# Performance work log

Measured on AMD Instinct MI355X. Metric: run time of the kernel, lower is better.

## Reference

```python
import jax, jax.numpy as jnp
import numpy as np

D_MODEL = 384
D_STATE = 64
N_LAYERS = 2
OUTPUT_DIM = 60
MAX_SEQ = 128
EXPAND = 2
D_CONV = 4
HEADDIM = 64
D_INNER = EXPAND * D_MODEL            # 768
NHEADS = D_INNER // HEADDIM           # 12
CONV_DIM = D_INNER + 2 * D_STATE      # 896
D_IN_PROJ = 2 * D_INNER + 2 * D_STATE + NHEADS  # 1676
BATCH = 256
SEQ = 128
EPS = 1e-5


def _pos_encoding(seq_len, d_model):
    pos = np.arange(seq_len, dtype=np.float32)[:, None]
    div = np.exp(np.arange(0, d_model, 2, dtype=np.float32) * (-np.log(10000.0) / d_model))
    pe = np.zeros((seq_len, d_model), dtype=np.float32)
    pe[:, 0::2] = np.sin(pos * div)
    pe[:, 1::2] = np.cos(pos * div)
    return jnp.asarray(pe)


def setup_inputs() -> dict:
    key = jax.random.key(0)
    ks = jax.random.split(key, 16)
    f32 = jnp.float32
    inp = {}
    inp["memory_embeddings"] = jax.random.normal(ks[0], (BATCH, SEQ, D_MODEL), dtype=f32)
    # per-layer Mamba2 params, stacked over layers
    inp["in_proj_w"] = jax.random.normal(ks[1], (N_LAYERS, D_IN_PROJ, D_MODEL), dtype=f32) * 0.02
    inp["conv_w"] = jax.random.normal(ks[2], (N_LAYERS, CONV_DIM, D_CONV), dtype=f32) * 0.2
    inp["conv_b"] = jax.random.normal(ks[3], (N_LAYERS, CONV_DIM), dtype=f32) * 0.02
    inp["dt_bias"] = jax.random.normal(ks[4], (N_LAYERS, NHEADS), dtype=f32) * 0.5 - 4.0
    inp["A_log"] = jnp.log(jax.random.uniform(ks[5], (N_LAYERS, NHEADS), dtype=f32, minval=1.0, maxval=16.0))
    inp["D"] = jnp.ones((N_LAYERS, NHEADS), dtype=f32) + jax.random.normal(ks[6], (N_LAYERS, NHEADS), dtype=f32) * 0.1
    inp["mamba_norm_w"] = jnp.ones((N_LAYERS, D_INNER), dtype=f32)
    inp["out_proj_w"] = jax.random.normal(ks[7], (N_LAYERS, D_MODEL, D_INNER), dtype=f32) * 0.02
    # pre-Mamba LayerNorms
    inp["ln_w"] = jnp.ones((N_LAYERS, D_MODEL), dtype=f32)
    inp["ln_b"] = jnp.zeros((N_LAYERS, D_MODEL), dtype=f32)
    # output norm + projection
    inp["out_norm_w"] = jnp.ones((D_MODEL,), dtype=f32)
    inp["out_norm_b"] = jnp.zeros((D_MODEL,), dtype=f32)
    inp["proj_w"] = jax.random.normal(ks[8], (OUTPUT_DIM, D_MODEL), dtype=f32) * 0.05
    inp["proj_b"] = jnp.zeros((OUTPUT_DIM,), dtype=f32)
    return inp


def _layernorm(x, w, b):
    mu = jnp.mean(x, axis=-1, keepdims=True)
    var = jnp.mean(jnp.square(x - mu), axis=-1, keepdims=True)
    return (x - mu) * jax.lax.rsqrt(var + EPS) * w + b


def _silu(x):
    return x * jax.nn.sigmoid(x)


def _mamba2_block(x, in_proj_w, conv_w, conv_b, dt_bias, A_log, D, norm_w, out_proj_w):
    b, l, _ = x.shape
    zxbcdt = jnp.einsum('bld,ed->ble', x, in_proj_w)  # (b,l,1676)
    z = zxbcdt[..., :D_INNER]
    xBC = zxbcdt[..., D_INNER:D_INNER + CONV_DIM]
    dt = jax.nn.softplus(zxbcdt[..., -NHEADS:] + dt_bias)  # (b,l,h)
    # depthwise causal conv1d (kernel 4) + silu
    xp = jnp.pad(xBC, ((0, 0), (D_CONV - 1, 0), (0, 0)))
    xconv = conv_b
    for k in range(D_CONV):
        xconv = xconv + xp[:, k:k + l, :] * conv_w[:, k]
    xBC = _silu(xconv)
    xh = xBC[..., :D_INNER].reshape(b, l, NHEADS, HEADDIM)  # (b,l,h,p)
    Bm = xBC[..., D_INNER:D_INNER + D_STATE]                # (b,l,n)
    Cm = xBC[..., D_INNER + D_STATE:]                       # (b,l,n)
    A = -jnp.exp(A_log)  # (h,)

    def step(h, inp):
        x_t, B_t, C_t, dt_t = inp  # (b,h,p), (b,n), (b,n), (b,h)
        dA = jnp.exp(dt_t * A)  # (b,h)
        h = h * dA[..., None, None] + jnp.einsum('bh,bhp,bn->bhpn', dt_t, x_t, B_t)
        y = jnp.einsum('bhpn,bn->bhp', h, C_t)
        return h, y

    h0 = jnp.zeros((b, NHEADS, HEADDIM, D_STATE), dtype=x.dtype)
    xs = (xh.transpose(1, 0, 2, 3), Bm.transpose(1, 0, 2), Cm.transpose(1, 0, 2), dt.transpose(1, 0, 2))
    _, ys = jax.lax.scan(step, h0, xs)          # ys: (l,b,h,p)
    y = ys.transpose(1, 0, 2, 3) + D[None, None, :, None] * xh
    y = y.reshape(b, l, D_INNER)
    # gated RMSNorm (norm_before_gate=False): rmsnorm(y * silu(z)) * weight
    g = y * _silu(z)
    g = g * jax.lax.rsqrt(jnp.mean(jnp.square(g), axis=-1, keepdims=True) + EPS) * norm_w
    return jnp.einsum('ble,de->bld', g, out_proj_w)


def reference(memory_embeddings, in_proj_w, conv_w, conv_b, dt_bias, A_log, D,
              mamba_norm_w, out_proj_w, ln_w, ln_b, out_norm_w, out_norm_b,
              proj_w, proj_b):
    b, l, d = memory_embeddings.shape
    pe = _pos_encoding(MAX_SEQ, D_MODEL)[:l]
    x = memory_embeddings + pe[None]  # dropout is identity at eval
    for i in range(N_LAYERS):
        residual = x
        xn = _layernorm(x, ln_w[i], ln_b[i])
        xm = _mamba2_block(xn, in_proj_w[i], conv_w[i], conv_b[i], dt_bias[i],
                           A_log[i], D[i], mamba_norm_w[i], out_proj_w[i])
        x = xm + residual
    x = _layernorm(x, out_norm_w, out_norm_b)
    final = x[:, -1, :]  # (b, d_model)
    return final @ proj_w.T + proj_b  # (b, output_dim)
```

## Files before the change

### kernel.cpp

```cpp
#include <hip/hip_runtime.h>
#include <math.h>

#define BATCH   256
#define SEQ     128
#define DMODEL  384
#define DSTATE  64
#define DINNER  768
#define NHEADS  12
#define HEADDIM 64
#define CONVDIM 896
#define DPROJ   1676
#define N1PAD   1792
#define OUTDIM  60
#define MTOT    (BATCH*SEQ)

typedef unsigned short u16;
typedef unsigned int   u32;
typedef short bf16x8 __attribute__((ext_vector_type(8)));
typedef float f32x4 __attribute__((ext_vector_type(4)));

#define ASG __attribute__((address_space(1)))
#define ASL __attribute__((address_space(3)))

__device__ __forceinline__ float siluf(float x){ return __fdividef(x, 1.f + __expf(-x)); }
__device__ __forceinline__ float softplusf(float x){ return fmaxf(x,0.f) + log1pf(expf(-fabsf(x))); }
__device__ __forceinline__ u16 f2bf(float x){
  union { float f; unsigned int u; } c; c.f = x;
  unsigned int r = c.u + 0x7FFFu + ((c.u >> 16) & 1u);
  return (u16)(r >> 16);
}
__device__ __forceinline__ float bf2f(u16 u){
  union { unsigned int u; float f; } c; c.u = ((unsigned int)u) << 16;
  return c.f;
}

__global__ void add_pe_kernel(const float* __restrict__ emb, float* __restrict__ x){
  int idx = blockIdx.x*256 + threadIdx.x;
  int d = idx % DMODEL;
  int l = (idx / DMODEL) % SEQ;
  int i = d >> 1;
  float div = expf((float)(2*i) * (-9.210340371976184f/384.f));
  float arg = (float)l * div;
  float pe = (d & 1) ? cosf(arg) : sinf(arg);
  x[idx] = emb[idx] + pe;
}

__global__ void wconv_in2_kernel(const float* __restrict__ w, u16* __restrict__ o){
  int idx = blockIdx.x*256 + threadIdx.x;
  int n = idx / DMODEL, k = idx % DMODEL;
  o[idx] = (n < DPROJ) ? f2bf(w[(size_t)n*DMODEL + k]) : (u16)0;
}
__global__ void wconv_out_kernel(const float* __restrict__ w, u16* __restrict__ o){
  int idx = blockIdx.x*256 + threadIdx.x;
  o[idx] = f2bf(w[idx]);
}

__global__ void __launch_bounds__(256) ln_bf_kernel(const float* __restrict__ x,
    const float* __restrict__ lnw, const float* __restrict__ lnb, u16* __restrict__ xbf){
  int wave = threadIdx.x >> 6, lane = threadIdx.x & 63;
  int m = blockIdx.x*4 + wave;
  const float* row = x + (size_t)m*DMODEL;
  float v[6], s=0.f, s2=0.f;
  #pragma unroll
  for (int j=0;j<6;j++){ v[j] = row[lane + 64*j]; s += v[j]; s2 += v[j]*v[j]; }
  #pragma unroll
  for (int off=32;off;off>>=1){ s += __shfl_xor(s,off,64); s2 += __shfl_xor(s2,off,64); }
  float m1 = s * (1.f/384.f);
  float var = s2 * (1.f/384.f) - m1*m1;
  float rstd = rsqrtf(var + 1e-5f);
  u16* orow = xbf + (size_t)m*DMODEL;
  #pragma unroll
  for (int j=0;j<6;j++){
    int d = lane + 64*j;
    orow[d] = f2bf((v[j]-m1)*rstd*lnw[d] + lnb[d]);
  }
}

template<int MODE>
__global__ void __launch_bounds__(256) gemm_bf16(
    const u16* __restrict__ A, const u16* __restrict__ W, const int K,
    u16* __restrict__ zo, u16* __restrict__ xbcro, float* __restrict__ dto,
    const float* __restrict__ dt_bias, float* __restrict__ xres)
{
  __shared__ __align__(16) u16 As[2*128*32];
  __shared__ __align__(16) u16 Bs[2*128*32];
  const int tid = threadIdx.x;
  const int l = tid & 63;
  const int w = tid >> 6;
  const int wm = w >> 1, wn = w & 1;

  int bx = blockIdx.x, by = blockIdx.y;
  {
    const int nwg = gridDim.x * gridDim.y;
    if ((nwg & 7) == 0){
      const int id  = by * gridDim.x + bx;
      const int nid = (id & 7) * (nwg >> 3) + (id >> 3);
      bx = nid % gridDim.x;
      by = nid / gridDim.x;
    }
  }
  const int m0 = by * 128, n0 = bx * 128;

  f32x4 acc[4][4];
  #pragma unroll
  for (int i=0;i<4;i++)
    #pragma unroll
    for (int j=0;j<4;j++)
      acc[i][j] = (f32x4){0.f,0.f,0.f,0.f};

  const int grow = tid >> 2;
  const int gcol = (tid & 3) * 8;
  const u16* Abase = A + (size_t)(m0 + grow)*K + gcol;
  const u16* Wbase = W + (size_t)(n0 + grow)*K + gcol;
  const int lb = w*512;

  auto stage = [&](int buf, int k0){
    #pragma unroll
    for (int it=0; it<2; it++){
      __builtin_amdgcn_global_load_lds((const ASG void*)(Abase + (size_t)it*64*K + k0),
                                       (ASL void*)(&As[buf*4096 + it*2048 + lb]), 16, 0, 0);
      __builtin_amdgcn_global_load_lds((const ASG void*)(Wbase + (size_t)it*64*K + k0),
                                       (ASL void*)(&Bs[buf*4096 + it*2048 + lb]), 16, 0, 0);
    }
  };

  const int nt = K >> 5;
  stage(0, 0);
  const int rr = l & 15;
  const int ko = (l >> 4) << 3;
  for (int t = 0; t < nt; t++){
    if (t + 1 < nt){
      stage((t+1)&1, (t+1)<<5);
      asm volatile("s_waitcnt vmcnt(4)" ::: "memory");
    } else {
      asm volatile("s_waitcnt vmcnt(0)" ::: "memory");
    }
    __builtin_amdgcn_s_barrier();
    __builtin_amdgcn_sched_barrier(0);
    const u16* Ac = &As[(t&1)*4096];
    const u16* Bc = &Bs[(t&1)*4096];
    bf16x8 af[4], bfv[4];
    #pragma unroll
    for (int f=0; f<4; f++){
      af[f]  = *(const bf16x8*)&Ac[(wm*64 + f*16 + rr)*32 + ko];
      bfv[f] = *(const bf16x8*)&Bc[(wn*64 + f*16 + rr)*32 + ko];
    }
    #pragma unroll
    for (int fi=0; fi<4; fi++)
      #pragma unroll
      for (int fj=0; fj<4; fj++)
        acc[fi][fj] = __builtin_amdgcn_mfma_f32_16x16x32_bf16(af[fi], bfv[fj], acc[fi][fj], 0, 0, 0);
    asm volatile("s_waitcnt lgkmcnt(0)" ::: "memory");
    __builtin_amdgcn_sched_barrier(0);
    __builtin_amdgcn_s_barrier();
  }

  const int cg = l & 15;
  const int rb = (l >> 4) * 4;
  #pragma unroll
  for (int fi=0; fi<4; fi++){
    #pragma unroll
    for (int r=0; r<4; r++){
      const int m = m0 + wm*64 + fi*16 + rb + r;
      #pragma unroll
      for (int fj=0; fj<4; fj++){
        const int n = n0 + wn*64 + fj*16 + cg;
        float v = acc[fi][fj][r];
        if (MODE == 0){
          if (n < DINNER)            zo[(size_t)m*DINNER + n] = f2bf(v);
          else if (n < DINNER+CONVDIM) xbcro[(size_t)m*CONVDIM + n - DINNER] = f2bf(v);
          else if (n < DPROJ)        dto[(size_t)m*NHEADS + n - (DINNER+CONVDIM)] =
                                        softplusf(v + dt_bias[n - (DINNER+CONVDIM)]);
        } else {
          xres[(size_t)m*DMODEL + n] += v;
        }
      }
    }
  }
}

__global__ void __launch_bounds__(256) conv_bc_kernel(
    const u16* __restrict__ xbcr, const float* __restrict__ cw,
    const float* __restrict__ cb, u16* __restrict__ xbcc)
{
  int idx = blockIdx.x*256 + threadIdx.x;
  int row = idx >> 4;
  int c8  = (idx & 15) * 8;
  int lq  = row & (SEQ-1);
  const u16* src = xbcr + (size_t)row*CONVDIM + DINNER + c8;
  bf16x8 tap[4];
  #pragma unroll
  for (int k=0;k<4;k++){
    int d = k - 3;
    if (lq + d >= 0) tap[k] = *(const bf16x8*)(src + (long)d*CONVDIM);
    else             tap[k] = (bf16x8){0,0,0,0,0,0,0,0};
  }
  bf16x8 o;
  #pragma unroll
  for (int j=0;j<8;j++){
    const float4 wv = *(const float4*)&cw[(DINNER + c8 + j)*4];
    float a = cb[DINNER + c8 + j]
            + bf2f((u16)tap[0][j])*wv.x + bf2f((u16)tap[1][j])*wv.y
            + bf2f((u16)tap[2][j])*wv.z + bf2f((u16)tap[3][j])*wv.w;
    o[j] = (short)f2bf(siluf(a));
  }
  *(bf16x8*)&xbcc[(size_t)row*128 + c8] = o;
}

__global__ void __launch_bounds__(256) ssd_kernel(
  const u16* __restrict__ xbcr, const u16* __restrict__ xbcc,
  const float* __restrict__ dtb,
  const float* __restrict__ cw, const float* __restrict__ cb,
  const float* __restrict__ A_log, const float* __restrict__ Dp,
  u16* __restrict__ y)
{
  const int b = blockIdx.x, h = blockIdx.y;
  const int tid = threadIdx.x;
  const int l = tid & 63;
  const int w = tid >> 6;
  const float A  = -__expf(A_log[h]);
  const float Dh = Dp[h];

  __shared__ __align__(16) u16 cbm[128*128];
  __shared__ __align__(16) u16 XtS[64*128];
  __shared__ float cum[128];
  __shared__ float dts[128];
  char* Cb = (char*)cbm;
  char* Bb = (char*)cbm + 16384;
  char* Mb = (char*)cbm;
  char* Xb = (char*)XtS;

  const u16* xrow  = xbcr + (size_t)b*SEQ*CONVDIM;
  const u16* ccrow = xbcc + (size_t)b*SEQ*128;

  if (w == 0){
    float a0 = dtb[((size_t)b*SEQ + 2*l)*NHEADS + h];
    float a1 = dtb[((size_t)b*SEQ + 2*l+1)*NHEADS + h];
    float ps = (a0 + a1) * A;
    #pragma unroll
    for (int off=1; off<64; off<<=1){
      float v = __shfl_up(ps, off, 64);
      if (l >= off) ps += v;
    }
    float excl = ps - (a0 + a1)*A;
    cum[2*l]   = excl + a0*A;
    cum[2*l+1] = ps;
    dts[2*l]   = a0;
    dts[2*l+1] = a1;
  }

  {
    const int row0 = tid >> 4;
    const int colc = (tid & 15) * 8;
    #pragma unroll
    for (int it=0; it<8; it++){
      const int r = row0 + 16*it;
      bf16x8 v = *(const bf16x8*)&ccrow[(size_t)r*128 + colc];
      if (colc < 64) *(bf16x8*)(Bb + ((r*128 + 2*colc)      ^ ((r&7)<<4))) = v;
      else           *(bf16x8*)(Cb + ((r*128 + 2*(colc-64)) ^ ((r&7)<<4))) = v;
    }
  }

  {
    const int cx = h*HEADDIM + l;
    const float4 cwx = *(const float4*)&cw[cx*4];
    const float cbx = cb[cx];
    const int sb = 32*w;
    float p3=0.f, p2=0.f, p1=0.f;
    if (w > 0){
      p3 = bf2f(xrow[(size_t)(sb-3)*CONVDIM + cx]);
      p2 = bf2f(xrow[(size_t)(sb-2)*CONVDIM + cx]);
      p1 = bf2f(xrow[(size_t)(sb-1)*CONVDIM + cx]);
    }
    #pragma unroll
    for (int it=0; it<16; it++){
      const int s = sb + 2*it;
      const float r0 = bf2f(xrow[(size_t)s*CONVDIM + cx]);
      const float r1 = bf2f(xrow[(size_t)(s+1)*CONVDIM + cx]);
      const float v0 = siluf(cbx + p3*cwx.x + p2*cwx.y + p1*cwx.z + r0*cwx.w);
      const float v1 = siluf(cbx + p2*cwx.x + p1*cwx.y + r0*cwx.z + r1*cwx.w);
      const u32 pk = (u32)f2bf(v0) | ((u32)f2bf(v1) << 16);
      *(u32*)(Xb + ((l*256 + 2*s) ^ ((l&7)<<4))) = pk;
      p3 = p1; p2 = r0; p1 = r1;
    }
  }
  __syncthreads();

  const int t0 = w*32;
  const int rr = l & 15;
  const int kg = (l >> 4) << 3;
  f32x4 g[2][8];
  #pragma unroll
  for (int i=0;i<2;i++)
    #pragma unroll
    for (int j=0;j<8;j++)
      g[i][j] = (f32x4){0.f,0.f,0.f,0.f};
  #pragma unroll
  for (int k0=0; k0<64; k0+=32){
    const int ko = k0 + kg;
    bf16x8 af[2], bfv[8];
    #pragma unroll
    for (int fi=0; fi<2; fi++){
      const int r = t0 + 16*fi + rr;
      af[fi] = *(const bf16x8*)(Cb + ((r*128 + 2*ko) ^ ((r&7)<<4)));
    }
    #pragma unroll
    for (int fj=0; fj<8; fj++){
      const int r = 16*fj + rr;
      bfv[fj] = *(const bf16x8*)(Bb + ((r*128 + 2*ko) ^ ((r&7)<<4)));
    }
    #pragma unroll
    for (int fi=0; fi<2; fi++)
      #pragma unroll
      for (int fj=0; fj<8; fj++)
        g[fi][fj] = __builtin_amdgcn_mfma_f32_16x16x32_bf16(af[fi], bfv[fj], g[fi][fj], 0, 0, 0);
  }
  __syncthreads();

  {
    const int rowg = (l >> 4) * 4;
    const int colg = l & 15;
    #pragma unroll
    for (int fi=0; fi<2; fi++){
      #pragma unroll
      for (int fj=0; fj<8; fj++){
        const int s = 16*fj + colg;
        const float cs = cum[s];
        const float ds = dts[s];
        #pragma unroll
        for (int r=0; r<4; r++){
          const int t = t0 + 16*fi + rowg + r;
          float m = 0.f;
          if (t >= s) m = __expf(cum[t] - cs) * ds * g[fi][fj][r];
          *(u16*)(Mb + ((t*256 + 2*s) ^ ((t&7)<<4))) = f2bf(m);
        }
      }
    }
  }
  __syncthreads();

  f32x4 acc[2][4];
  #pragma unroll
  for (int i=0;i<2;i++)
    #pragma unroll
    for (int j=0;j<4;j++)
      acc[i][j] = (f32x4){0.f,0.f,0.f,0.f};
  #pragma unroll
  for (int k0=0; k0<128; k0+=32){
    const int ko = k0 + kg;
    bf16x8 af[2], bfv[4];
    #pragma unroll
    for (int fi=0; fi<2; fi++){
      const int r = t0 + 16*fi + rr;
      af[fi] = *(const bf16x8*)(Mb + ((r*256 + 2*ko) ^ ((r&7)<<4)));
    }
    #pragma unroll
    for (int fj=0; fj<4; fj++){
      const int r = 16*fj + rr;
      bfv[fj] = *(const bf16x8*)(Xb + ((r*256 + 2*ko) ^ ((r&7)<<4)));
    }
    #pragma unroll
    for (int fi=0; fi<2; fi++)
      #pragma unroll
      for (int fj=0; fj<4; fj++)
        acc[fi][fj] = __builtin_amdgcn_mfma_f32_16x16x32_bf16(af[fi], bfv[fj], acc[fi][fj], 0, 0, 0);
  }

  {
    const int rowg = (l >> 4) * 4;
    const int colg = l & 15;
    u16* yb = y + (size_t)b*SEQ*DINNER + h*HEADDIM;
    #pragma unroll
    for (int fi=0; fi<2; fi++){
      #pragma unroll
      for (int r=0; r<4; r++){
        const int t = t0 + 16*fi + rowg + r;
        #pragma unroll
        for (int fj=0; fj<4; fj++){
          const int p = 16*fj + colg;
          const float xval = bf2f(*(const u16*)(Xb + ((p*256 + 2*t) ^ ((p&7)<<4))));
          yb[(size_t)t*DINNER + p] = f2bf(acc[fi][fj][r] + Dh*xval);
        }
      }
    }
  }
}

__global__ void __launch_bounds__(192) gate_rms_bf_kernel(const u16* __restrict__ z,
    const float* __restrict__ normw, u16* __restrict__ y){
  const int m = blockIdx.x, tid = threadIdx.x;
  const uint2 zz = *(const uint2*)(z + (size_t)m*DINNER + tid*4);
  const uint2 yy = *(const uint2*)(y + (size_t)m*DINNER + tid*4);
  float gv[4];
  gv[0] = bf2f((u16)(yy.x & 0xffff)) * siluf(bf2f((u16)(zz.x & 0xffff)));
  gv[1] = bf2f((u16)(yy.x >> 16))    * siluf(bf2f((u16)(zz.x >> 16)));
  gv[2] = bf2f((u16)(yy.y & 0xffff)) * siluf(bf2f((u16)(zz.y & 0xffff)));
  gv[3] = bf2f((u16)(yy.y >> 16))    * siluf(bf2f((u16)(zz.y >> 16)));
  float ss = gv[0]*gv[0] + gv[1]*gv[1] + gv[2]*gv[2] + gv[3]*gv[3];
  #pragma unroll
  for (int off=32;off;off>>=1) ss += __shfl_xor(ss,off,64);
  __shared__ float red[3];
  if ((tid&63)==0) red[tid>>6] = ss;
  __syncthreads();
  const float rms = rsqrtf((red[0]+red[1]+red[2])*(1.f/768.f) + 1e-5f);
  const float4 nw = *(const float4*)(normw + tid*4);
  u32 o0 = (u32)f2bf(gv[0]*rms*nw.x) | ((u32)f2bf(gv[1]*rms*nw.y) << 16);
  u32 o1 = (u32)f2bf(gv[2]*rms*nw.z) | ((u32)f2bf(gv[3]*rms*nw.w) << 16);
  *(uint2*)(y + (size_t)m*DINNER + tid*4) = make_uint2(o0, o1);
}

__global__ void __launch_bounds__(64) final_kernel(const float* __restrict__ x,
  const float* __restrict__ onw, const float* __restrict__ onb,
  const float* __restrict__ pw, const float* __restrict__ pb, float* __restrict__ out)
{
  int b = blockIdx.x;
  int lane = threadIdx.x;
  const float* row = x + ((size_t)b*SEQ + (SEQ-1))*DMODEL;
  float s=0.f, s2=0.f;
  float v[6];
  #pragma unroll
  for (int j=0;j<6;j++){ v[j] = row[lane + 64*j]; s += v[j]; s2 += v[j]*v[j]; }
  #pragma unroll
  for (int off=32;off;off>>=1){ s += __shfl_xor(s,off,64); s2 += __shfl_xor(s2,off,64); }
  float m1 = s*(1.f/384.f);
  float var = s2*(1.f/384.f) - m1*m1;
  float rstd = rsqrtf(var + 1e-5f);
  __shared__ float xn[384];
  #pragma unroll
  for (int j=0;j<6;j++){
    int d = lane + 64*j;
    xn[d] = (v[j]-m1)*rstd*onw[d] + onb[d];
  }
  __syncthreads();
  if (lane < OUTDIM){
    const float* wrow = pw + lane*DMODEL;
    float acc = pb[lane];
    #pragma unroll 4
    for (int d=0; d<DMODEL; d+=4){
      float4 xv = *(const float4*)&xn[d];
      float4 wv = *(const float4*)&wrow[d];
      acc += xv.x*wv.x + xv.y*wv.y + xv.z*wv.z + xv.w*wv.w;
    }
    out[b*OUTDIM + lane] = acc;
  }
}

extern "C" void kernel_launch(void* const* d_in, const int* in_sizes, int n_in,
                              void* d_out, int out_size, void* d_ws, size_t ws_size,
                              hipStream_t stream){
  const float* emb        = (const float*)d_in[0];
  const float* in_proj_w  = (const float*)d_in[1];
  const float* conv_w     = (const float*)d_in[2];
  const float* conv_b     = (const float*)d_in[3];
  const float* dt_bias    = (const float*)d_in[4];
  const float* A_log      = (const float*)d_in[5];
  const float* Dp         = (const float*)d_in[6];
  const float* mnw        = (const float*)d_in[7];
  const float* out_proj_w = (const float*)d_in[8];
  const float* ln_w       = (const float*)d_in[9];
  const float* ln_b       = (const float*)d_in[10];
  const float* onw        = (const float*)d_in[11];
  const float* onb        = (const float*)d_in[12];
  const float* pw         = (const float*)d_in[13];
  const float* pb         = (const float*)d_in[14];
  float* out = (float*)d_out;

  const size_t XB    = (size_t)MTOT*DMODEL*4;
  const size_t XBFB  = (size_t)MTOT*DMODEL*2;
  const size_t WINB  = (size_t)N1PAD*DMODEL*2;
  const size_t WOUTB = (size_t)DMODEL*DINNER*2;
  const size_t fixed = XB + XBFB + WINB + WOUTB;
  int CB = 256;
  while (CB > 1 && fixed + (size_t)CB*SEQ*5168ull > ws_size) CB >>= 1;
  const int Mc = CB*SEQ;
  const int nchunks = BATCH / CB;

  char* p = (char*)d_ws;
  float* x      = (float*)p;  p += XB;
  u16*   xbf    = (u16*)p;    p += XBFB;
  u16*   wbfin  = (u16*)p;    p += WINB;
  u16*   wbfout = (u16*)p;    p += WOUTB;
  u16*   z      = (u16*)p;    p += (size_t)Mc*DINNER*2;
  u16*   xbcr   = (u16*)p;    p += (size_t)Mc*CONVDIM*2;
  u16*   xbcc   = (u16*)p;    p += (size_t)Mc*128*2;
  float* dt     = (float*)p;  p += (size_t)Mc*NHEADS*4;
  u16*   y      = (u16*)p;

  add_pe_kernel<<<MTOT*DMODEL/256,256,0,stream>>>(emb, x);
  for (int i=0;i<2;i++){
    wconv_in2_kernel<<<N1PAD*DMODEL/256,256,0,stream>>>(in_proj_w + (size_t)i*DPROJ*DMODEL, wbfin);
    wconv_out_kernel<<<DMODEL*DINNER/256,256,0,stream>>>(out_proj_w + (size_t)i*DMODEL*DINNER, wbfout);
    ln_bf_kernel<<<MTOT/4,256,0,stream>>>(x, ln_w + (size_t)i*DMODEL, ln_b + (size_t)i*DMODEL, xbf);
    for (int c=0;c<nchunks;c++){
      const u16* ac = xbf + (size_t)c*Mc*DMODEL;
      float*     xc = x   + (size_t)c*Mc*DMODEL;
      dim3 g1(N1PAD/128, Mc/128);
      gemm_bf16<0><<<g1,256,0,stream>>>(ac, wbfin, DMODEL, z, xbcr, dt,
                                        dt_bias + (size_t)i*NHEADS, nullptr);
      conv_bc_kernel<<<Mc/16,256,0,stream>>>(xbcr, conv_w + (size_t)i*CONVDIM*4,
                                             conv_b + (size_t)i*CONVDIM, xbcc);
      dim3 gs(CB, NHEADS);
      ssd_kernel<<<gs,256,0,stream>>>(xbcr, xbcc, dt,
          conv_w + (size_t)i*CONVDIM*4, conv_b + (size_t)i*CONVDIM,
          A_log + (size_t)i*NHEADS, Dp + (size_t)i*NHEADS, y);
      gate_rms_bf_kernel<<<Mc,192,0,stream>>>(z, mnw + (size_t)i*DINNER, y);
      dim3 g2(DMODEL/128, Mc/128);
      gemm_bf16<1><<<g2,256,0,stream>>>(y, wbfout, DINNER, nullptr, nullptr, nullptr, nullptr, xc);
    }
  }
  final_kernel<<<BATCH,64,0,stream>>>(x, onw, onb, pw, pb, out);
}
```

Before: 545.8 us.

## Switch GEMM to single-wave 64x64 tiles with XOR-swizzled LDS, no barriers

The bf16 MFMA GEMM goes from 256-thread workgroups with 128x128 tiles to one wave per workgroup computing a 64x64 tile. Because only one wave touches the LDS buffers, the s_barrier calls are removed. The LDS layout gets an XOR swizzle on both the load and read side to avoid bank conflicts. The grid grows fourfold, so each A and W element is reused less and global/L2 traffic rises in exchange for more parallelism and no synchronisation.

```diff
diff --git a/kernel.cpp b/kernel.cpp
--- a/kernel.cpp
+++ b/kernel.cpp
@@ -77,17 +77,14 @@
 }
 
 template<int MODE>
-__global__ void __launch_bounds__(256) gemm_bf16(
+__global__ void __launch_bounds__(64) gemm_bf16(
     const u16* __restrict__ A, const u16* __restrict__ W, const int K,
     u16* __restrict__ zo, u16* __restrict__ xbcro, float* __restrict__ dto,
     const float* __restrict__ dt_bias, float* __restrict__ xres)
 {
-  __shared__ __align__(16) u16 As[2*128*32];
-  __shared__ __align__(16) u16 Bs[2*128*32];
-  const int tid = threadIdx.x;
-  const int l = tid & 63;
-  const int w = tid >> 6;
-  const int wm = w >> 1, wn = w & 1;
+  __shared__ __align__(16) u16 As[2*64*32];
+  __shared__ __align__(16) u16 Bs[2*64*32];
+  const int l = threadIdx.x;
 
   int bx = blockIdx.x, by = blockIdx.y;
   {
@@ -99,7 +96,7 @@
       by = nid / gridDim.x;
     }
   }
-  const int m0 = by * 128, n0 = bx * 128;
+  const int m0 = by * 64, n0 = bx * 64;
 
   f32x4 acc[4][4];
   #pragma unroll
@@ -108,42 +105,42 @@
     for (int j=0;j<4;j++)
       acc[i][j] = (f32x4){0.f,0.f,0.f,0.f};
 
-  const int grow = tid >> 2;
-  const int gcol = (tid & 3) * 8;
-  const u16* Abase = A + (size_t)(m0 + grow)*K + gcol;
-  const u16* Wbase = W + (size_t)(n0 + grow)*K + gcol;
-  const int lb = w*512;
+  const int r0s = ((l>>2)&1) ^ ((l>>4)&1);
+  const int rA  = 2*(l>>3) + r0s;
+  const int cbA = (l&3) ^ ((2*((l>>3)&1) + r0s) & 3);
+  const u16* Asrc = A + (size_t)(m0 + rA)*K + cbA*8;
+  const u16* Wsrc = W + (size_t)(n0 + rA)*K + cbA*8;
 
   auto stage = [&](int buf, int k0){
     #pragma unroll
-    for (int it=0; it<2; it++){
-      __builtin_amdgcn_global_load_lds((const ASG void*)(Abase + (size_t)it*64*K + k0),
-                                       (ASL void*)(&As[buf*4096 + it*2048 + lb]), 16, 0, 0);
-      __builtin_amdgcn_global_load_lds((const ASG void*)(Wbase + (size_t)it*64*K + k0),
-                                       (ASL void*)(&Bs[buf*4096 + it*2048 + lb]), 16, 0, 0);
+    for (int it=0; it<4; it++){
+      __builtin_amdgcn_global_load_lds((const ASG void*)(Asrc + (size_t)it*16*K + k0),
+                                       (ASL void*)(&As[buf*2048 + it*512]), 16, 0, 0);
+      __builtin_amdgcn_global_load_lds((const ASG void*)(Wsrc + (size_t)it*16*K + k0),
+                                       (ASL void*)(&Bs[buf*2048 + it*512]), 16, 0, 0);
     }
   };
 
   const int nt = K >> 5;
   stage(0, 0);
   const int rr = l & 15;
-  const int ko = (l >> 4) << 3;
+  const int kb = (l >> 4) * 16;
+  const int sw = (rr & 7) << 4;
   for (int t = 0; t < nt; t++){
     if (t + 1 < nt){
       stage((t+1)&1, (t+1)<<5);
-      asm volatile("s_waitcnt vmcnt(4)" ::: "memory");
+      asm volatile("s_waitcnt vmcnt(8)" ::: "memory");
     } else {
       asm volatile("s_waitcnt vmcnt(0)" ::: "memory");
     }
-    __builtin_amdgcn_s_barrier();
     __builtin_amdgcn_sched_barrier(0);
-    const u16* Ac = &As[(t&1)*4096];
-    const u16* Bc = &Bs[(t&1)*4096];
+    const char* Ab = (const char*)As + (t&1)*4096;
+    const char* Bb = (const char*)Bs + (t&1)*4096;
     bf16x8 af[4], bfv[4];
     #pragma unroll
     for (int f=0; f<4; f++){
-      af[f]  = *(const bf16x8*)&Ac[(wm*64 + f*16 + rr)*32 + ko];
-      bfv[f] = *(const bf16x8*)&Bc[(wn*64 + f*16 + rr)*32 + ko];
+      af[f]  = *(const bf16x8*)(Ab + (((f*16+rr)*64 + kb) ^ sw));
+      bfv[f] = *(const bf16x8*)(Bb + (((f*16+rr)*64 + kb) ^ sw));
     }
     #pragma unroll
     for (int fi=0; fi<4; fi++)
@@ -152,7 +149,6 @@
         acc[fi][fj] = __builtin_amdgcn_mfma_f32_16x16x32_bf16(af[fi], bfv[fj], acc[fi][fj], 0, 0, 0);
     asm volatile("s_waitcnt lgkmcnt(0)" ::: "memory");
     __builtin_amdgcn_sched_barrier(0);
-    __builtin_amdgcn_s_barrier();
   }
 
   const int cg = l & 15;
@@ -161,10 +157,10 @@
   for (int fi=0; fi<4; fi++){
     #pragma unroll
     for (int r=0; r<4; r++){
-      const int m = m0 + wm*64 + fi*16 + rb + r;
+      const int m = m0 + fi*16 + rb + r;
       #pragma unroll
       for (int fj=0; fj<4; fj++){
-        const int n = n0 + wn*64 + fj*16 + cg;
+        const int n = n0 + fj*16 + cg;
         float v = acc[fi][fj][r];
         if (MODE == 0){
           if (n < DINNER)            zo[(size_t)m*DINNER + n] = f2bf(v);
@@ -494,9 +490,9 @@
     for (int c=0;c<nchunks;c++){
       const u16* ac = xbf + (size_t)c*Mc*DMODEL;
       float*     xc = x   + (size_t)c*Mc*DMODEL;
-      dim3 g1(N1PAD/128, Mc/128);
-      gemm_bf16<0><<<g1,256,0,stream>>>(ac, wbfin, DMODEL, z, xbcr, dt,
-                                        dt_bias + (size_t)i*NHEADS, nullptr);
+      dim3 g1(N1PAD/64, Mc/64);
+      gemm_bf16<0><<<g1,64,0,stream>>>(ac, wbfin, DMODEL, z, xbcr, dt,
+                                       dt_bias + (size_t)i*NHEADS, nullptr);
       conv_bc_kernel<<<Mc/16,256,0,stream>>>(xbcr, conv_w + (size_t)i*CONVDIM*4,
                                              conv_b + (size_t)i*CONVDIM, xbcc);
       dim3 gs(CB, NHEADS);
@@ -504,8 +500,8 @@
           conv_w + (size_t)i*CONVDIM*4, conv_b + (size_t)i*CONVDIM,
           A_log + (size_t)i*NHEADS, Dp + (size_t)i*NHEADS, y);
       gate_rms_bf_kernel<<<Mc,192,0,stream>>>(z, mnw + (size_t)i*DINNER, y);
-      dim3 g2(DMODEL/128, Mc/128);
-      gemm_bf16<1><<<g2,256,0,stream>>>(y, wbfout, DINNER, nullptr, nullptr, nullptr, nullptr, xc);
+      dim3 g2(DMODEL/64, Mc/64);
+      gemm_bf16<1><<<g2,64,0,stream>>>(y, wbfout, DINNER, nullptr, nullptr, nullptr, nullptr, xc);
     }
   }
   final_kernel<<<BATCH,64,0,stream>>>(x, onw, onb, pw, pb, out);
```

After: 621.6 us. 1.14x slower.
